# Optimization experiments

Measured on AMD Instinct MI355X. Metric: run time of the kernel, lower is better.

Reference implementation:

```python
import jax, jax.numpy as jnp
import numpy as np

B, N_IN, N_LATENT, STEPS = 256, 1024, 128, 256


def setup_inputs() -> dict:
    key = jax.random.key(0)
    kx, kf, kt = jax.random.split(key, 3)
    x = jax.random.normal(kx, (B, N_IN), dtype=jnp.float32)
    # transform ~ N(0, 0.1) per module's initialize_weights
    transform = 0.1 * jax.random.normal(kf, (N_IN, N_LATENT), dtype=jnp.float32)
    # transition scaled so spectral radius ~0.9 (std*sqrt(n_latent) ~ 0.9)
    # to keep the 256-step linear recurrence numerically stable
    transition = (0.9 / np.sqrt(N_LATENT)) * jax.random.normal(
        kt, (N_LATENT, N_LATENT), dtype=jnp.float32)
    return {"x": x, "transform": transform, "transition": transition,
            "steps": STEPS}


def reference(x, transform, transition, steps):
    # x: [B, n_in] -> latent0: [B, n_latent]
    latent0 = x @ transform

    def step(lat, _):
        lat = lat @ transition  # [B, n_latent]
        return lat, lat

    # lats: [steps, B, n_latent] -- latent states AFTER each transition
    _, lats = jax.lax.scan(step, latent0, None, length=steps)
    # project all latent states back to data space in one contraction
    # out[b, n, s] = sum_l lats[s, b, l] * transform[n, l]
    out = jnp.einsum('sbl,nl->bns', lats, transform)  # [B, n_in, steps]
    return out
```

## Files before the change

kernel.cpp:

```cpp
#include <hip/hip_runtime.h>
#include <hip/hip_bf16.h>

#define NIN 1024
#define NL 128
#define CMS 32768
#define MAGIC 0x4D474331

typedef __attribute__((ext_vector_type(8))) short bf16x8_t;
typedef __attribute__((ext_vector_type(4))) float f32x4_t;

__device__ inline unsigned short f2bf(float f) {
    __hip_bfloat16 h = __float2bfloat16(f);
    return *reinterpret_cast<unsigned short*>(&h);
}
__device__ inline float bf2f(unsigned short u) {
    unsigned int x = (unsigned int)u << 16;
    return __uint_as_float(x);
}
__device__ inline ushort4 pack4(f32x4_t v) {
    ushort4 o;
    o.x = f2bf(v[0]); o.y = f2bf(v[1]); o.z = f2bf(v[2]); o.w = f2bf(v[3]);
    return o;
}


__device__ __forceinline__ void stageBT(const float* __restrict__ Bg,
                                        unsigned short* BtHi, unsigned short* BtLo) {
    int t = threadIdx.x;
    for (int idx = t; idx < 4096; idx += 256) {
        int l = idx >> 5, c4 = (idx & 31) * 4;
        f32x4_t v = *(const f32x4_t*)&Bg[(size_t)l * 128 + c4];
#pragma unroll
        for (int q = 0; q < 4; ++q) {
            int c = c4 + q;
            float f = v[q];
            unsigned short hi = f2bf(f);
            unsigned short lo = f2bf(f - bf2f(hi));
            int byt = c * 256 + ((2 * l) ^ ((c & 7) << 4));
            *(unsigned short*)((char*)BtHi + byt) = hi;
            *(unsigned short*)((char*)BtLo + byt) = lo;
        }
    }
}

__device__ __forceinline__ void stageBT_T(const float* __restrict__ Btr,
                                          unsigned short* BtHi, unsigned short* BtLo) {
    int t = threadIdx.x;
    for (int idx = t; idx < 4096; idx += 256) {
        int c = idx >> 5, l4 = (idx & 31) * 4;
        f32x4_t v = *(const f32x4_t*)&Btr[(size_t)c * 128 + l4];
        ushort4 hi, lo;
        hi.x = f2bf(v[0]); lo.x = f2bf(v[0] - bf2f(hi.x));
        hi.y = f2bf(v[1]); lo.y = f2bf(v[1] - bf2f(hi.y));
        hi.z = f2bf(v[2]); lo.z = f2bf(v[2] - bf2f(hi.z));
        hi.w = f2bf(v[3]); lo.w = f2bf(v[3] - bf2f(hi.w));
        int byt = c * 256 + ((2 * l4) ^ ((c & 7) << 4));
        *(ushort4*)((char*)BtHi + byt) = hi;
        *(ushort4*)((char*)BtLo + byt) = lo;
    }
}

__device__ __forceinline__ void loadX(const float* __restrict__ Ag, float* X) {
    int t = threadIdx.x;
    for (int idx = t; idx < 1024; idx += 256) {
        int rr = idx >> 5, c4 = (idx & 31) * 4;
        f32x4_t v = *(const f32x4_t*)&Ag[(size_t)rr * 128 + c4];
        *(f32x4_t*)((char*)X + rr * 512 + ((c4 * 4) ^ ((rr & 7) << 4))) = v;
    }
}

__device__ __forceinline__ void chainStage(const float* X, float* Xn,
                                           const unsigned short* BtHi,
                                           const unsigned short* BtLo) {
    int t = threadIdx.x, w = t >> 6, lane = t & 63;
    int r = lane & 15, g = lane >> 4;
    int rt = w & 1, ctb = (w >> 1) * 4;
    int rr = rt * 16 + r;
    int sw = (rr & 7) << 4;
    bf16x8_t avHi[4], avLo[4];
#pragma unroll
    for (int kk = 0; kk < 4; ++kk) {
        int c0 = (kk * 4 + g) * 8;
        f32x4_t x0 = *(const f32x4_t*)((const char*)X + rr * 512 + ((c0 * 4) ^ sw));
        f32x4_t x1 = *(const f32x4_t*)((const char*)X + rr * 512 + (((c0 + 4) * 4) ^ sw));
        bf16x8_t hi, lo;
#pragma unroll
        for (int q = 0; q < 4; ++q) {
            unsigned short h0 = f2bf(x0[q]);
            hi[q] = (short)h0;
            lo[q] = (short)f2bf(x0[q] - bf2f(h0));
            unsigned short h1 = f2bf(x1[q]);
            hi[4 + q] = (short)h1;
            lo[4 + q] = (short)f2bf(x1[q] - bf2f(h1));
        }
        avHi[kk] = hi; avLo[kk] = lo;
    }
#pragma unroll
    for (int ct = 0; ct < 4; ++ct) {
        int cb = (ctb + ct) * 16 + r;
        int swb = (cb & 7) << 4;
        f32x4_t acc = (f32x4_t){0.f, 0.f, 0.f, 0.f};
#pragma unroll
        for (int kk = 0; kk < 4; ++kk) {
            int lb2 = (kk * 4 + g) * 16;
            int byt = cb * 256 + (lb2 ^ swb);
            bf16x8_t bh = *(const bf16x8_t*)((const char*)BtHi + byt);
            bf16x8_t bl = *(const bf16x8_t*)((const char*)BtLo + byt);
            acc = __builtin_amdgcn_mfma_f32_16x16x32_bf16(bh, avHi[kk], acc, 0, 0, 0);
            acc = __builtin_amdgcn_mfma_f32_16x16x32_bf16(bh, avLo[kk], acc, 0, 0, 0);
            acc = __builtin_amdgcn_mfma_f32_16x16x32_bf16(bl, avHi[kk], acc, 0, 0, 0);
        }
        int cc = (ctb + ct) * 16 + g * 4;
        *(f32x4_t*)((char*)Xn + rr * 512 + ((cc * 4) ^ sw)) = acc;
    }
}

__device__ __forceinline__ void writeXf(const float* X, float* __restrict__ Df) {
    int t = threadIdx.x;
    for (int idx = t; idx < 1024; idx += 256) {
        int rr = idx >> 5, c4 = (idx & 31) * 4;
        f32x4_t v = *(const f32x4_t*)((const char*)X + rr * 512 + ((c4 * 4) ^ ((rr & 7) << 4)));
        *(f32x4_t*)&Df[(size_t)rr * 128 + c4] = v;
    }
}

__device__ __forceinline__ void writeXbf(const float* X,
                                         unsigned short* __restrict__ base, int rstride) {
    int t = threadIdx.x;
    for (int idx = t; idx < 1024; idx += 256) {
        int rr = idx >> 5, c4 = (idx & 31) * 4;
        f32x4_t v = *(const f32x4_t*)((const char*)X + rr * 512 + ((c4 * 4) ^ ((rr & 7) << 4)));
        *(ushort4*)&base[(size_t)rr * rstride + c4] = pack4(v);
    }
}

__global__ __launch_bounds__(256) void k_pre(const float* __restrict__ x,
                                             const float* __restrict__ tf,
                                             const float* __restrict__ tr,
                                             float* __restrict__ T16f,
                                             float* __restrict__ Cf,
                                             unsigned short* __restrict__ Cc,
                                             unsigned short* __restrict__ H,
                                             int* __restrict__ cells) {
    __shared__ __align__(16) char lds[98304];
    unsigned short* BtHi = (unsigned short*)lds;
    unsigned short* BtLo = (unsigned short*)(lds + 32768);
    float* X0 = (float*)(lds + 65536);
    float* X1 = (float*)(lds + 65536 + 16384);
    int blk = blockIdx.x, t = threadIdx.x;

    if (blk < 32) {
        float* xr = (float*)lds;
        int b0 = blk * 8;
        for (int idx = t; idx < 2048; idx += 256) {
            int rr = idx >> 8, c = idx & 255;
            ((float4*)xr)[rr * 256 + c] =
                ((const float4*)(x + (size_t)(b0 + rr) * NIN))[c];
        }
        __syncthreads();
        int cg = t & 31, rs = t >> 5;
        const float* xp = xr + rs * NIN;
        f32x4_t acc = (f32x4_t){0.f, 0.f, 0.f, 0.f};
#pragma unroll 8
        for (int i = 0; i < NIN; ++i) {
            f32x4_t tv = *(const f32x4_t*)&tf[i * NL + cg * 4];
            acc += xp[i] * tv;
        }
        int row = b0 + rs;
        *(f32x4_t*)&Cf[(size_t)row * NL + cg * 4] = acc;
        *(ushort4*)&Cc[(size_t)row * NL + cg * 4] = pack4(acc);
        __syncthreads();
        if (t == 0)
            __hip_atomic_store(&cells[blk], MAGIC, __ATOMIC_RELEASE,
                               __HIP_MEMORY_SCOPE_AGENT);
    } else if (blk < 36) {
        int r0 = (blk - 32) * 32;
        stageBT(tr, BtHi, BtLo);
        loadX(tr + (size_t)r0 * NL, X0);
        __syncthreads();
        float* cur = X0; float* nxt = X1;
        for (int s = 0; s < 15; ++s) {
            chainStage(cur, nxt, BtHi, BtLo);
            __syncthreads();
            float* tmp = cur; cur = nxt; nxt = tmp;
        }
        writeXf(cur, T16f + (size_t)r0 * NL);
        __syncthreads();
        if (t == 0)
            __hip_atomic_store(&cells[blk], MAGIC, __ATOMIC_RELEASE,
                               __HIP_MEMORY_SCOPE_AGENT);
    } else if (blk < 68) {
        int n0 = (blk - 36) * 32;
        stageBT_T(tr, BtHi, BtLo);
        loadX(tf + (size_t)n0 * NL, X0);
        __syncthreads();
        float* cur = X0; float* nxt = X1;
        for (int s = 1; s <= 16; ++s) {
            chainStage(cur, nxt, BtHi, BtLo);
            __syncthreads();
            writeXbf(nxt, H + ((size_t)n0 * 16 + (s - 1)) * NL, 16 * NL);
            float* tmp = cur; cur = nxt; nxt = tmp;
        }
    } else {
        int cb = blk - 68, r0 = cb * 32;
        if (t == 0) {
#pragma unroll
            for (int q = 0; q < 8; ++q) {
                int ci = (q < 4) ? (cb * 4 + q) : (32 + q - 4);
                for (int it = 0; it < (1 << 22); ++it) {
                    if (__hip_atomic_load(&cells[ci], __ATOMIC_ACQUIRE,
                                          __HIP_MEMORY_SCOPE_AGENT) == MAGIC)
                        break;
                    __builtin_amdgcn_s_sleep(2);
                }
            }
            __threadfence();
        }
        __syncthreads();
        stageBT(T16f, BtHi, BtLo);
        loadX(Cf + (size_t)r0 * NL, X0);
        __syncthreads();
        float* cur = X0; float* nxt = X1;
        for (int j = 1; j <= 15; ++j) {
            chainStage(cur, nxt, BtHi, BtLo);
            __syncthreads();
            writeXbf(nxt, Cc + (size_t)j * CMS + (size_t)r0 * NL, NL);
            float* tmp = cur; cur = nxt; nxt = tmp;
        }
    }
}

__global__ __launch_bounds__(256) void k_main(const unsigned short* __restrict__ Cc,
                                              const unsigned short* __restrict__ H,
                                              float* __restrict__ out) {
    int bid = blockIdx.x;
    int e = ((bid & 7) << 7) | (bid >> 3);
    int ct = e >> 3, bt = (e >> 2) & 1, jq = e & 3;
    __shared__ __align__(16) char lds[49152];
    char* lB = lds;
    int t = threadIdx.x;
    const unsigned short* Bg = H + (size_t)(ct * 128) * NL;
    for (int i = t; i < 2048; i += 256) {
        int row = i >> 4, c = i & 15;
        int sw = (c * 16) ^ ((row & 7) << 4);
        *(bf16x8_t*)(lB + row * 256 + sw) =
            *(const bf16x8_t*)(Bg + (size_t)row * NL + c * 8);
    }
    __syncthreads();
    int w = t >> 6, lane = t & 63;
    int wr = (w >> 1) * 64;
    int wc = (w & 1) * 64;
    int r = lane & 15, g = lane >> 4;
    char* slab = lds + 32768 + w * 4096;

    for (int mf = 0; mf < 4; ++mf) {
        int brow_base = bt * 128 + wr + mf * 16;
        bf16x8_t av[4][4];
#pragma unroll
        for (int jj4 = 0; jj4 < 4; ++jj4) {
            int j = jq * 4 + jj4;
            const unsigned short* Arow =
                Cc + (size_t)j * CMS + (size_t)(brow_base + r) * NL;
#pragma unroll
            for (int kk = 0; kk < 4; ++kk)
                av[jj4][kk] = *(const bf16x8_t*)(Arow + (kk * 4 + g) * 8);
        }
        for (int nf = 0; nf < 4; ++nf) {
            int nn = (w & 1) * 4 + nf;
            int rowB = wc + nf * 16 + r;
            bf16x8_t bvv[4];
#pragma unroll
            for (int kk = 0; kk < 4; ++kk)
                bvv[kk] = *(const bf16x8_t*)(
                    lB + rowB * 256 + (((kk * 4 + g) * 16) ^ ((rowB & 7) << 4)));
            f32x4_t acc4[4];
#pragma unroll
            for (int q = 0; q < 4; ++q) acc4[q] = (f32x4_t){0.f, 0.f, 0.f, 0.f};
#pragma unroll
            for (int jj4 = 0; jj4 < 4; ++jj4)
#pragma unroll
                for (int kk = 0; kk < 4; ++kk)
                    acc4[jj4] = __builtin_amdgcn_mfma_f32_16x16x32_bf16(
                        bvv[kk], av[jj4][kk], acc4[jj4], 0, 0, 0);
#pragma unroll
            for (int jj4 = 0; jj4 < 4; ++jj4) {
                int boff = r * 256 + ((jj4 * 64 + g * 16 + r * 32) & 255);
                *(f32x4_t*)(slab + boff) = acc4[jj4];
            }
#pragma unroll
            for (int i2 = 0; i2 < 4; ++i2) {
                int lin = i2 * 1024 + lane * 16;
                int rs = lin >> 8, cb = lin & 255;
                f32x4_t v = *(const f32x4_t*)(slab + rs * 256 + ((cb + rs * 32) & 255));
                size_t o = (size_t)(brow_base + rs) * (NIN * 256) +
                           (size_t)(ct * 8 + nn) * 256 + jq * 64 + (cb >> 2);
                *(f32x4_t*)&out[o] = v;
            }
        }
    }
}

extern "C" void kernel_launch(void* const* d_in, const int* in_sizes, int n_in,
                              void* d_out, int out_size, void* d_ws, size_t ws_size,
                              hipStream_t stream) {
    const float* x = (const float*)d_in[0];
    const float* tf = (const float*)d_in[1];
    const float* tr = (const float*)d_in[2];
    float* out = (float*)d_out;

    float* T16f = (float*)d_ws;
    float* Cf = T16f + 16384;
    unsigned short* Cc = (unsigned short*)(Cf + (size_t)256 * NL);
    unsigned short* H = Cc + (size_t)16 * CMS;
    int* cells = (int*)(H + (size_t)16384 * NL);

    k_pre<<<76, 256, 0, stream>>>(x, tf, tr, T16f, Cf, Cc, H, cells);
    k_main<<<1024, 256, 0, stream>>>(Cc, H, out);
}
```

Measured before the change: 105.1 us.

## Shorten k_pre serial chain with power-doubling and odd/even split

Replaces the 15-step serial chain that built T^16 with T^4 computed first, followed by repeated squaring-style products yielding T^16 and T^32. The 15-step latent chain is split across even and odd lanes of blocks, each running 7 steps with T^32. The aim is to cut the critical-path length of the pre-kernel, which runs on few blocks. This adds more cross-block spin-wait dependencies, more workspace and more blocks, and changes rounding because more matrix powers are composed.

```diff
diff --git a/kernel.cpp b/kernel.cpp
--- a/kernel.cpp
+++ b/kernel.cpp
@@ -22,7 +22,6 @@
     o.x = f2bf(v[0]); o.y = f2bf(v[1]); o.z = f2bf(v[2]); o.w = f2bf(v[3]);
     return o;
 }
-
 
 __device__ __forceinline__ void stageBT(const float* __restrict__ Bg,
                                         unsigned short* BtHi, unsigned short* BtLo) {
@@ -134,11 +133,31 @@
     }
 }
 
+__device__ __forceinline__ void signal(int* cells, int ci) {
+    __syncthreads();
+    if (threadIdx.x == 0)
+        __hip_atomic_store(&cells[ci], MAGIC, __ATOMIC_RELEASE,
+                           __HIP_MEMORY_SCOPE_AGENT);
+}
+__device__ __forceinline__ void waitRange(int* cells, int c0, int n) {
+    for (int q = 0; q < n; ++q) {
+        for (int it = 0; it < (1 << 22); ++it) {
+            if (__hip_atomic_load(&cells[c0 + q], __ATOMIC_ACQUIRE,
+                                  __HIP_MEMORY_SCOPE_AGENT) == MAGIC)
+                break;
+            __builtin_amdgcn_s_sleep(2);
+        }
+    }
+}
+
 __global__ __launch_bounds__(256) void k_pre(const float* __restrict__ x,
                                              const float* __restrict__ tf,
                                              const float* __restrict__ tr,
+                                             float* __restrict__ T4f,
                                              float* __restrict__ T16f,
+                                             float* __restrict__ T32f,
                                              float* __restrict__ Cf,
+                                             float* __restrict__ Cf1,
                                              unsigned short* __restrict__ Cc,
                                              unsigned short* __restrict__ H,
                                              int* __restrict__ cells) {
@@ -169,28 +188,95 @@
         int row = b0 + rs;
         *(f32x4_t*)&Cf[(size_t)row * NL + cg * 4] = acc;
         *(ushort4*)&Cc[(size_t)row * NL + cg * 4] = pack4(acc);
-        __syncthreads();
-        if (t == 0)
-            __hip_atomic_store(&cells[blk], MAGIC, __ATOMIC_RELEASE,
-                               __HIP_MEMORY_SCOPE_AGENT);
+        signal(cells, blk);
     } else if (blk < 36) {
         int r0 = (blk - 32) * 32;
         stageBT(tr, BtHi, BtLo);
         loadX(tr + (size_t)r0 * NL, X0);
         __syncthreads();
         float* cur = X0; float* nxt = X1;
-        for (int s = 0; s < 15; ++s) {
-            chainStage(cur, nxt, BtHi, BtLo);
-            __syncthreads();
-            float* tmp = cur; cur = nxt; nxt = tmp;
-        }
-        writeXf(cur, T16f + (size_t)r0 * NL);
-        __syncthreads();
-        if (t == 0)
-            __hip_atomic_store(&cells[blk], MAGIC, __ATOMIC_RELEASE,
-                               __HIP_MEMORY_SCOPE_AGENT);
-    } else if (blk < 68) {
-        int n0 = (blk - 36) * 32;
+        for (int s = 0; s < 3; ++s) {
+            chainStage(cur, nxt, BtHi, BtLo);
+            __syncthreads();
+            float* tmp = cur; cur = nxt; nxt = tmp;
+        }
+        writeXf(cur, T4f + (size_t)r0 * NL);
+        signal(cells, blk);
+    } else if (blk < 40) {
+        int i = blk - 36, r0 = i * 32;
+        if (t == 0) { waitRange(cells, 32, 4); __threadfence(); }
+        __syncthreads();
+        stageBT(T4f, BtHi, BtLo);
+        loadX(T4f + (size_t)r0 * NL, X0);
+        __syncthreads();
+        float* cur = X0; float* nxt = X1;
+        for (int s = 1; s <= 7; ++s) {
+            chainStage(cur, nxt, BtHi, BtLo);
+            __syncthreads();
+            if (s == 3) {
+                writeXf(nxt, T16f + (size_t)r0 * NL);
+                signal(cells, 36 + i);
+            }
+            if (s == 7) {
+                writeXf(nxt, T32f + (size_t)r0 * NL);
+                signal(cells, 40 + i);
+            }
+            float* tmp = cur; cur = nxt; nxt = tmp;
+        }
+    } else if (blk < 48) {
+        int cb = blk - 40, r0 = cb * 32;
+        if (t == 0) {
+            waitRange(cells, 36, 4);
+            waitRange(cells, cb * 4, 4);
+            __threadfence();
+        }
+        __syncthreads();
+        stageBT(T16f, BtHi, BtLo);
+        loadX(Cf + (size_t)r0 * NL, X0);
+        __syncthreads();
+        chainStage(X0, X1, BtHi, BtLo);
+        __syncthreads();
+        writeXf(X1, Cf1 + (size_t)r0 * NL);
+        writeXbf(X1, Cc + (size_t)CMS + (size_t)r0 * NL, NL);
+        signal(cells, 44 + cb);
+    } else if (blk < 56) {
+        int cb = blk - 48, r0 = cb * 32;
+        if (t == 0) {
+            waitRange(cells, 40, 4);
+            waitRange(cells, cb * 4, 4);
+            __threadfence();
+        }
+        __syncthreads();
+        stageBT(T32f, BtHi, BtLo);
+        loadX(Cf + (size_t)r0 * NL, X0);
+        __syncthreads();
+        float* cur = X0; float* nxt = X1;
+        for (int k = 1; k <= 7; ++k) {
+            chainStage(cur, nxt, BtHi, BtLo);
+            __syncthreads();
+            writeXbf(nxt, Cc + (size_t)(2 * k) * CMS + (size_t)r0 * NL, NL);
+            float* tmp = cur; cur = nxt; nxt = tmp;
+        }
+    } else if (blk < 64) {
+        int cb = blk - 56, r0 = cb * 32;
+        if (t == 0) {
+            waitRange(cells, 40, 4);
+            waitRange(cells, 44 + cb, 1);
+            __threadfence();
+        }
+        __syncthreads();
+        stageBT(T32f, BtHi, BtLo);
+        loadX(Cf1 + (size_t)r0 * NL, X0);
+        __syncthreads();
+        float* cur = X0; float* nxt = X1;
+        for (int k = 1; k <= 7; ++k) {
+            chainStage(cur, nxt, BtHi, BtLo);
+            __syncthreads();
+            writeXbf(nxt, Cc + (size_t)(1 + 2 * k) * CMS + (size_t)r0 * NL, NL);
+            float* tmp = cur; cur = nxt; nxt = tmp;
+        }
+    } else {
+        int n0 = (blk - 64) * 32;
         stageBT_T(tr, BtHi, BtLo);
         loadX(tf + (size_t)n0 * NL, X0);
         __syncthreads();
@@ -199,32 +285,6 @@
             chainStage(cur, nxt, BtHi, BtLo);
             __syncthreads();
             writeXbf(nxt, H + ((size_t)n0 * 16 + (s - 1)) * NL, 16 * NL);
-            float* tmp = cur; cur = nxt; nxt = tmp;
-        }
-    } else {
-        int cb = blk - 68, r0 = cb * 32;
-        if (t == 0) {
-#pragma unroll
-            for (int q = 0; q < 8; ++q) {
-                int ci = (q < 4) ? (cb * 4 + q) : (32 + q - 4);
-                for (int it = 0; it < (1 << 22); ++it) {
-                    if (__hip_atomic_load(&cells[ci], __ATOMIC_ACQUIRE,
-                                          __HIP_MEMORY_SCOPE_AGENT) == MAGIC)
-                        break;
-                    __builtin_amdgcn_s_sleep(2);
-                }
-            }
-            __threadfence();
-        }
-        __syncthreads();
-        stageBT(T16f, BtHi, BtLo);
-        loadX(Cf + (size_t)r0 * NL, X0);
-        __syncthreads();
-        float* cur = X0; float* nxt = X1;
-        for (int j = 1; j <= 15; ++j) {
-            chainStage(cur, nxt, BtHi, BtLo);
-            __syncthreads();
-            writeXbf(nxt, Cc + (size_t)j * CMS + (size_t)r0 * NL, NL);
             float* tmp = cur; cur = nxt; nxt = tmp;
         }
     }
@@ -308,12 +368,15 @@
     const float* tr = (const float*)d_in[2];
     float* out = (float*)d_out;
 
-    float* T16f = (float*)d_ws;
-    float* Cf = T16f + 16384;
-    unsigned short* Cc = (unsigned short*)(Cf + (size_t)256 * NL);
+    float* T4f = (float*)d_ws;
+    float* T16f = T4f + 16384;
+    float* T32f = T16f + 16384;
+    float* Cf = T32f + 16384;
+    float* Cf1 = Cf + (size_t)256 * NL;
+    unsigned short* Cc = (unsigned short*)(Cf1 + (size_t)256 * NL);
     unsigned short* H = Cc + (size_t)16 * CMS;
     int* cells = (int*)(H + (size_t)16384 * NL);
 
-    k_pre<<<76, 256, 0, stream>>>(x, tf, tr, T16f, Cf, Cc, H, cells);
+    k_pre<<<96, 256, 0, stream>>>(x, tf, tr, T4f, T16f, T32f, Cf, Cf1, Cc, H, cells);
     k_main<<<1024, 256, 0, stream>>>(Cc, H, out);
 }
```

New measurement: 105.8 us. About the same (+0.7%).
